# Kernel optimization log

Measured on AMD Instinct MI355X. Metric: run time of the kernel, lower is better.

Reference implementation:

```python
import jax, jax.numpy as jnp
import numpy as np

B, T, I, H = 256, 2048, 128, 128

def setup_inputs() -> dict:
    key = jax.random.key(0)
    k = jax.random.split(key, 5)
    bound = 1.0 / np.sqrt(H)  # torch RNNCell init: U(-1/sqrt(H), 1/sqrt(H))
    return {
        "x": jax.random.normal(k[0], (B, T, I), dtype=jnp.float32),
        "weight_ih": jax.random.uniform(k[1], (H, I), jnp.float32, -bound, bound),
        "weight_hh": jax.random.uniform(k[2], (H, H), jnp.float32, -bound, bound),
        "bias_ih": jax.random.uniform(k[3], (H,), jnp.float32, -bound, bound),
        "bias_hh": jax.random.uniform(k[4], (H,), jnp.float32, -bound, bound),
    }

def reference(x, weight_ih, weight_hh, bias_ih, bias_hh):
    # Tanh RNN: h_t = tanh(x_t @ W_ih^T + b_ih + h_{t-1} @ W_hh^T + b_hh)
    # Precompute the input projection for all timesteps (one big GEMM),
    # then scan the recurrent part (sequential dependency on h).
    b = x.shape[0]
    h0 = jnp.zeros((b, weight_hh.shape[0]), dtype=x.dtype)
    # [B, T, H]
    x_proj = jnp.einsum('bti,hi->bth', x, weight_ih) + bias_ih + bias_hh

    def step(h, xt):  # xt: [B, H]
        h_new = jnp.tanh(xt + h @ weight_hh.T)
        return h_new, h_new

    _, out = jax.lax.scan(step, h0, jnp.swapaxes(x_proj, 0, 1))  # out: [T, B, H]
    return jnp.swapaxes(out, 0, 1)  # [B, T, H]
```

## Files before the change

### kernel.cpp

```cpp
#include <hip/hip_runtime.h>

#define BB 256
#define TT 2048
#define II 128
#define HH 128
#define GS 16
#define NG (TT / GS)

typedef __attribute__((ext_vector_type(8))) short short8;
typedef __attribute__((ext_vector_type(4))) float f32x4;

__device__ __forceinline__ void step_barrier() {
    asm volatile("s_waitcnt lgkmcnt(0)\n\ts_barrier" ::: "memory");
}

__device__ __forceinline__ float tanh_fast(float s) {
#if __has_builtin(__builtin_amdgcn_exp2f)
    const float e = __builtin_amdgcn_exp2f(s * 2.8853900817779268f);
#else
    const float e = exp2f(s * 2.8853900817779268f);
#endif
    return 1.0f - 2.0f * __builtin_amdgcn_rcpf(e + 1.0f);
}

__device__ __forceinline__ unsigned int f2bf(float f) {
    unsigned int u = __float_as_uint(f);
    u += 0x7FFF + ((u >> 16) & 1);
    return u >> 16;
}
__device__ __forceinline__ unsigned int cvtpk(float a, float b) {
    unsigned int r;
    asm("v_cvt_pk_bf16_f32 %0, %1, %2" : "=v"(r) : "v"(a), "v"(b));
    return r;
}

__launch_bounds__(512, 1)
__global__ void rnn_pipe(const float* __restrict__ x,
                         const float* __restrict__ w_ih,
                         const float* __restrict__ w_hh,
                         const float* __restrict__ b_ih,
                         const float* __restrict__ b_hh,
                         float* __restrict__ out) {
    const int b    = blockIdx.x;
    const int tid  = threadIdx.x;
    const int wave = tid >> 6;
    const int lane = tid & 63;
    const bool hw  = (wave < 4);

    __shared__ __align__(16) unsigned short hA[2][HH];
    __shared__ __align__(16) float axbuf[3][GS][HH];
    __shared__ __align__(16) unsigned short xstage[2][4][64][8];

    const float* xb = x + (size_t)b * (TT * II);
    const f32x4 z4 = {0.f, 0.f, 0.f, 0.f};

    const int jb_h = (wave & 3) * 32;
    short8 WH[2][4];
    if (hw) {
#pragma unroll
        for (int nt = 0; nt < 2; ++nt) {
            const int jj = jb_h + nt * 16 + (lane & 15);
#pragma unroll
            for (int kf = 0; kf < 4; ++kf) {
                short8 s;
#pragma unroll
                for (int e = 0; e < 8; ++e) {
                    const int kp = kf * 32 + (lane >> 4) * 8 + e;
                    const int mm = kp & 31;
                    const int ko = (kp & ~31) + (mm >> 1) + ((mm & 1) << 4);
                    s[e] = (short)f2bf(w_hh[(size_t)jj * HH + ko]);
                }
                WH[nt][kf] = s;
            }
        }
    }

    const int xwq = wave - 4;
    const int jb  = xwq * 32;
    short8 WF[2][4];
    float biasv[2];
    f32x4 bs0 = z4, bs1 = z4;
    const int q   = tid - 256;
    const int t_s = q >> 4;
    const int m   = q & 15;
    const int i0  = m * 8;
    const int kfs = m >> 2;
    const int lps = (m & 3) * 16 + t_s;
    const int c16 = lane & 15;
    if (!hw) {
#pragma unroll
        for (int nt = 0; nt < 2; ++nt) {
            const int jj = jb + nt * 16 + (lane & 15);
            biasv[nt] = b_ih[jj] + b_hh[jj];
#pragma unroll
            for (int kf = 0; kf < 4; ++kf) {
                const float* wp = w_ih + (size_t)jj * II + kf * 32 + (lane >> 4) * 8;
                short8 s;
#pragma unroll
                for (int e = 0; e < 8; ++e) s[e] = (short)f2bf(wp[e]);
                WF[nt][kf] = s;
            }
        }
#pragma unroll
        for (int r = 0; r < 4; ++r) { bs0[r] = biasv[0]; bs1[r] = biasv[1]; }
    }

#define STAGE_X(BUF, R0, R1) do { \
        uint4 P_; \
        P_.x = cvtpk((R0).x, (R0).y); P_.y = cvtpk((R0).z, (R0).w); \
        P_.z = cvtpk((R1).x, (R1).y); P_.w = cvtpk((R1).z, (R1).w); \
        *reinterpret_cast<uint4*>(&xstage[BUF][kfs][lps][0]) = P_; } while (0)

#define XPROJ(SB, AB) do { \
        const short8 PA0 = *reinterpret_cast<const short8*>(&xstage[SB][0][lane][0]); \
        const short8 PA1 = *reinterpret_cast<const short8*>(&xstage[SB][1][lane][0]); \
        const short8 PA2 = *reinterpret_cast<const short8*>(&xstage[SB][2][lane][0]); \
        const short8 PA3 = *reinterpret_cast<const short8*>(&xstage[SB][3][lane][0]); \
        f32x4 ac0 = z4, ac1 = z4; \
        ac0 = __builtin_amdgcn_mfma_f32_16x16x32_bf16(PA0, WF[0][0], ac0, 0, 0, 0); \
        ac0 = __builtin_amdgcn_mfma_f32_16x16x32_bf16(PA1, WF[0][1], ac0, 0, 0, 0); \
        ac0 = __builtin_amdgcn_mfma_f32_16x16x32_bf16(PA2, WF[0][2], ac0, 0, 0, 0); \
        ac0 = __builtin_amdgcn_mfma_f32_16x16x32_bf16(PA3, WF[0][3], ac0, 0, 0, 0); \
        ac1 = __builtin_amdgcn_mfma_f32_16x16x32_bf16(PA0, WF[1][0], ac1, 0, 0, 0); \
        ac1 = __builtin_amdgcn_mfma_f32_16x16x32_bf16(PA1, WF[1][1], ac1, 0, 0, 0); \
        ac1 = __builtin_amdgcn_mfma_f32_16x16x32_bf16(PA2, WF[1][2], ac1, 0, 0, 0); \
        ac1 = __builtin_amdgcn_mfma_f32_16x16x32_bf16(PA3, WF[1][3], ac1, 0, 0, 0); \
        const int c_ = lane & 15, rb_ = (lane >> 4) * 4; \
        _Pragma("unroll") \
        for (int r = 0; r < 4; ++r) { \
            axbuf[AB][rb_ + r][jb + c_]      = ac0[r] + biasv[0]; \
            axbuf[AB][rb_ + r][jb + 16 + c_] = ac1[r] + biasv[1]; \
        } } while (0)

    float4 nr0, nr1;
    if (!hw) {
        float4 p0 = *reinterpret_cast<const float4*>(&xb[t_s * II + i0]);
        float4 p1 = *reinterpret_cast<const float4*>(&xb[t_s * II + i0 + 4]);
        STAGE_X(0, p0, p1);
    }
    if (tid < HH) hA[0][tid] = 0;
    __syncthreads();
    if (!hw) XPROJ(0, 0);
    __syncthreads();
    if (!hw) {
        float4 p0 = *reinterpret_cast<const float4*>(&xb[(GS + t_s) * II + i0]);
        float4 p1 = *reinterpret_cast<const float4*>(&xb[(GS + t_s) * II + i0 + 4]);
        STAGE_X(0, p0, p1);
    }
    __syncthreads();
    if (!hw) XPROJ(0, 1);
    __syncthreads();
    if (!hw) {
        float4 p0 = *reinterpret_cast<const float4*>(&xb[(2 * GS + t_s) * II + i0]);
        float4 p1 = *reinterpret_cast<const float4*>(&xb[(2 * GS + t_s) * II + i0 + 4]);
        STAGE_X(0, p0, p1);
        nr0 = *reinterpret_cast<const float4*>(&xb[(size_t)(3 * GS + t_s) * II + i0]);
        nr1 = *reinterpret_cast<const float4*>(&xb[(size_t)(3 * GS + t_s) * II + i0 + 4]);
    }
    __syncthreads();

    float axn0 = 0.f, axn1 = 0.f;
    f32x4 d00 = z4, d10 = z4;
    if (hw) {
        axn0 = axbuf[0][0][jb_h + c16];
        axn1 = axbuf[0][0][jb_h + 16 + c16];
        __builtin_amdgcn_s_setprio(1);
    }

    float* xout = nullptr;
    if (!hw && lane < 32) {
        xout = out + (size_t)b * (TT * HH) + jb + c16 + ((lane & 16) ? 16 : 0);
    }

    for (int g = 0; g < NG; ++g) {
        const int g3  = g % 3;
        const int g3n = (g + 1) % 3;
        const int g3x = (g + 2) % 3;
#pragma unroll
        for (int w = 0; w < GS; ++w) {
            if (hw) {
                const int p  = w & 1;
                const int ko = (lane >> 4) * 8;
                const short8 A0 = *reinterpret_cast<const short8*>(&hA[p][ 0 + ko]);
                const short8 A1 = *reinterpret_cast<const short8*>(&hA[p][32 + ko]);
                const short8 A2 = *reinterpret_cast<const short8*>(&hA[p][64 + ko]);
                const short8 A3 = *reinterpret_cast<const short8*>(&hA[p][96 + ko]);
                d00[0] = axn0;
                d10[0] = axn1;
                f32x4 e01, e02, e03, e11, e12, e13;
                d00 = __builtin_amdgcn_mfma_f32_16x16x32_bf16(A0, WH[0][0], d00, 0, 0, 0);
                e01 = __builtin_amdgcn_mfma_f32_16x16x32_bf16(A1, WH[0][1], z4,  0, 0, 0);
                e02 = __builtin_amdgcn_mfma_f32_16x16x32_bf16(A2, WH[0][2], z4,  0, 0, 0);
                e03 = __builtin_amdgcn_mfma_f32_16x16x32_bf16(A3, WH[0][3], z4,  0, 0, 0);
                d10 = __builtin_amdgcn_mfma_f32_16x16x32_bf16(A0, WH[1][0], d10, 0, 0, 0);
                e11 = __builtin_amdgcn_mfma_f32_16x16x32_bf16(A1, WH[1][1], z4,  0, 0, 0);
                e12 = __builtin_amdgcn_mfma_f32_16x16x32_bf16(A2, WH[1][2], z4,  0, 0, 0);
                e13 = __builtin_amdgcn_mfma_f32_16x16x32_bf16(A3, WH[1][3], z4,  0, 0, 0);
                {
                    const int wn  = (w + 1) & (GS - 1);
                    const int gnb = (w == GS - 1) ? g3n : g3;
                    axn0 = axbuf[gnb][wn][jb_h + c16];
                    axn1 = axbuf[gnb][wn][jb_h + 16 + c16];
                }
                const float s0 = (d00[0] + e01[0]) + (e02[0] + e03[0]);
                const float s1 = (d10[0] + e11[0]) + (e12[0] + e13[0]);
                const float hn0 = tanh_fast(s0);
                const float hn1 = tanh_fast(s1);
                const unsigned int hpk = cvtpk(hn0, hn1);
                if (lane < 16) {
                    *reinterpret_cast<unsigned int*>(&hA[p ^ 1][jb_h + 2 * lane]) = hpk;
                }
            } else {
                const int T = (g << 4) + w;
                if (T != 0 && lane < 32) {
                    const unsigned int rd = *reinterpret_cast<const unsigned int*>(
                        &hA[w & 1][jb + 2 * c16]);
                    const unsigned int v = (lane & 16) ? (rd & 0xffff0000u) : (rd << 16);
                    xout[(size_t)(T - 1) * HH] = __uint_as_float(v);
                }
                if (w == 14) {
                    if (g + 2 < NG) {
                        const short8 XA0 = *reinterpret_cast<const short8*>(&xstage[g & 1][0][lane][0]);
                        const short8 XA1 = *reinterpret_cast<const short8*>(&xstage[g & 1][1][lane][0]);
                        const short8 XA2 = *reinterpret_cast<const short8*>(&xstage[g & 1][2][lane][0]);
                        const short8 XA3 = *reinterpret_cast<const short8*>(&xstage[g & 1][3][lane][0]);
                        f32x4 xp0, xp1, xp2, xp3, yp0, yp1, yp2, yp3;
                        xp0 = __builtin_amdgcn_mfma_f32_16x16x32_bf16(XA0, WF[0][0], bs0, 0, 0, 0);
                        yp0 = __builtin_amdgcn_mfma_f32_16x16x32_bf16(XA0, WF[1][0], bs1, 0, 0, 0);
                        xp1 = __builtin_amdgcn_mfma_f32_16x16x32_bf16(XA1, WF[0][1], z4, 0, 0, 0);
                        yp1 = __builtin_amdgcn_mfma_f32_16x16x32_bf16(XA1, WF[1][1], z4, 0, 0, 0);
                        xp2 = __builtin_amdgcn_mfma_f32_16x16x32_bf16(XA2, WF[0][2], z4, 0, 0, 0);
                        yp2 = __builtin_amdgcn_mfma_f32_16x16x32_bf16(XA2, WF[1][2], z4, 0, 0, 0);
                        xp3 = __builtin_amdgcn_mfma_f32_16x16x32_bf16(XA3, WF[0][3], z4, 0, 0, 0);
                        yp3 = __builtin_amdgcn_mfma_f32_16x16x32_bf16(XA3, WF[1][3], z4, 0, 0, 0);
                        const f32x4 t0 = (xp0 + xp1) + (xp2 + xp3);
                        const f32x4 t1 = (yp0 + yp1) + (yp2 + yp3);
                        const int c_ = lane & 15, rb_ = (lane >> 4) * 4;
#pragma unroll
                        for (int r = 0; r < 4; ++r) {
                            axbuf[g3x][rb_ + r][jb + c_]      = t0[r];
                            axbuf[g3x][rb_ + r][jb + 16 + c_] = t1[r];
                        }
                    }
                    if (g + 3 < NG) {
                        STAGE_X((g + 1) & 1, nr0, nr1);
                    }
                    if (g + 4 < NG) {
                        const int tb = (g + 4) * GS;
                        nr0 = *reinterpret_cast<const float4*>(&xb[(size_t)(tb + t_s) * II + i0]);
                        nr1 = *reinterpret_cast<const float4*>(&xb[(size_t)(tb + t_s) * II + i0 + 4]);
                    }
                }
            }
            step_barrier();
        }
    }

    if (!hw && lane < 32) {
        const unsigned int rd = *reinterpret_cast<const unsigned int*>(
            &hA[0][jb + 2 * c16]);
        const unsigned int v = (lane & 16) ? (rd & 0xffff0000u) : (rd << 16);
        xout[(size_t)(TT - 1) * HH] = __uint_as_float(v);
    }
#undef XPROJ
#undef STAGE_X
}

extern "C" void kernel_launch(void* const* d_in, const int* in_sizes, int n_in,
                              void* d_out, int out_size, void* d_ws, size_t ws_size,
                              hipStream_t stream) {
    const float* x    = (const float*)d_in[0];
    const float* w_ih = (const float*)d_in[1];
    const float* w_hh = (const float*)d_in[2];
    const float* b_ih = (const float*)d_in[3];
    const float* b_hh = (const float*)d_in[4];
    float* out = (float*)d_out;

    rnn_pipe<<<BB, 512, 0, stream>>>(x, w_ih, w_hh, b_ih, b_hh, out);
}
```

Before: 464.7 us.

## Replicate hidden-state LDS buffer per row group and shrink projection pipeline depth

The hidden-state buffer is replicated four times, once per 16-lane row group, with padding. All lanes now write their packed bf16 h values into their own replica, and each row group reads only its own copy. The aim is to reduce LDS bank conflicts and broadcast contention on the serial recurrence's critical path. The x-projection ring buffer also shrinks from three to two stages, with the prologue and prefetch distances adjusted to match; this saves LDS but leaves less slack between the projection producer and the recurrent consumer.

```diff
diff --git a/kernel.cpp b/kernel.cpp
--- a/kernel.cpp
+++ b/kernel.cpp
@@ -6,6 +6,7 @@
 #define HH 128
 #define GS 16
 #define NG (TT / GS)
+#define HREP (HH + 8)
 
 typedef __attribute__((ext_vector_type(8))) short short8;
 typedef __attribute__((ext_vector_type(4))) float f32x4;
@@ -47,8 +48,8 @@
     const int lane = tid & 63;
     const bool hw  = (wave < 4);
 
-    __shared__ __align__(16) unsigned short hA[2][HH];
-    __shared__ __align__(16) float axbuf[3][GS][HH];
+    __shared__ __align__(16) unsigned short hAr[4][2][HREP];
+    __shared__ __align__(16) float axbuf[2][GS][HH];
     __shared__ __align__(16) unsigned short xstage[2][4][64][8];
 
     const float* xb = x + (size_t)b * (TT * II);
@@ -87,6 +88,7 @@
     const int kfs = m >> 2;
     const int lps = (m & 3) * 16 + t_s;
     const int c16 = lane & 15;
+    const int rg  = lane >> 4;
     if (!hw) {
 #pragma unroll
         for (int nt = 0; nt < 2; ++nt) {
@@ -136,26 +138,18 @@
     if (!hw) {
         float4 p0 = *reinterpret_cast<const float4*>(&xb[t_s * II + i0]);
         float4 p1 = *reinterpret_cast<const float4*>(&xb[t_s * II + i0 + 4]);
-        STAGE_X(0, p0, p1);
-    }
-    if (tid < HH) hA[0][tid] = 0;
-    __syncthreads();
-    if (!hw) XPROJ(0, 0);
+        STAGE_X(1, p0, p1);
+    }
+    for (int i = tid; i < 4 * 2 * HREP; i += 512)
+        ((unsigned short*)hAr)[i] = 0;
     __syncthreads();
     if (!hw) {
+        XPROJ(1, 0);
         float4 p0 = *reinterpret_cast<const float4*>(&xb[(GS + t_s) * II + i0]);
         float4 p1 = *reinterpret_cast<const float4*>(&xb[(GS + t_s) * II + i0 + 4]);
         STAGE_X(0, p0, p1);
-    }
-    __syncthreads();
-    if (!hw) XPROJ(0, 1);
-    __syncthreads();
-    if (!hw) {
-        float4 p0 = *reinterpret_cast<const float4*>(&xb[(2 * GS + t_s) * II + i0]);
-        float4 p1 = *reinterpret_cast<const float4*>(&xb[(2 * GS + t_s) * II + i0 + 4]);
-        STAGE_X(0, p0, p1);
-        nr0 = *reinterpret_cast<const float4*>(&xb[(size_t)(3 * GS + t_s) * II + i0]);
-        nr1 = *reinterpret_cast<const float4*>(&xb[(size_t)(3 * GS + t_s) * II + i0 + 4]);
+        nr0 = *reinterpret_cast<const float4*>(&xb[(size_t)(2 * GS + t_s) * II + i0]);
+        nr1 = *reinterpret_cast<const float4*>(&xb[(size_t)(2 * GS + t_s) * II + i0 + 4]);
     }
     __syncthreads();
 
@@ -173,18 +167,15 @@
     }
 
     for (int g = 0; g < NG; ++g) {
-        const int g3  = g % 3;
-        const int g3n = (g + 1) % 3;
-        const int g3x = (g + 2) % 3;
 #pragma unroll
         for (int w = 0; w < GS; ++w) {
             if (hw) {
                 const int p  = w & 1;
-                const int ko = (lane >> 4) * 8;
-                const short8 A0 = *reinterpret_cast<const short8*>(&hA[p][ 0 + ko]);
-                const short8 A1 = *reinterpret_cast<const short8*>(&hA[p][32 + ko]);
-                const short8 A2 = *reinterpret_cast<const short8*>(&hA[p][64 + ko]);
-                const short8 A3 = *reinterpret_cast<const short8*>(&hA[p][96 + ko]);
+                const int ko = rg * 8;
+                const short8 A0 = *reinterpret_cast<const short8*>(&hAr[rg][p][ 0 + ko]);
+                const short8 A1 = *reinterpret_cast<const short8*>(&hAr[rg][p][32 + ko]);
+                const short8 A2 = *reinterpret_cast<const short8*>(&hAr[rg][p][64 + ko]);
+                const short8 A3 = *reinterpret_cast<const short8*>(&hAr[rg][p][96 + ko]);
                 d00[0] = axn0;
                 d10[0] = axn1;
                 f32x4 e01, e02, e03, e11, e12, e13;
@@ -198,7 +189,7 @@
                 e13 = __builtin_amdgcn_mfma_f32_16x16x32_bf16(A3, WH[1][3], z4,  0, 0, 0);
                 {
                     const int wn  = (w + 1) & (GS - 1);
-                    const int gnb = (w == GS - 1) ? g3n : g3;
+                    const int gnb = (w == GS - 1) ? ((g + 1) & 1) : (g & 1);
                     axn0 = axbuf[gnb][wn][jb_h + c16];
                     axn1 = axbuf[gnb][wn][jb_h + 16 + c16];
                 }
@@ -207,19 +198,17 @@
                 const float hn0 = tanh_fast(s0);
                 const float hn1 = tanh_fast(s1);
                 const unsigned int hpk = cvtpk(hn0, hn1);
-                if (lane < 16) {
-                    *reinterpret_cast<unsigned int*>(&hA[p ^ 1][jb_h + 2 * lane]) = hpk;
-                }
+                *reinterpret_cast<unsigned int*>(&hAr[rg][p ^ 1][jb_h + 2 * c16]) = hpk;
             } else {
                 const int T = (g << 4) + w;
                 if (T != 0 && lane < 32) {
                     const unsigned int rd = *reinterpret_cast<const unsigned int*>(
-                        &hA[w & 1][jb + 2 * c16]);
+                        &hAr[0][w & 1][jb + 2 * c16]);
                     const unsigned int v = (lane & 16) ? (rd & 0xffff0000u) : (rd << 16);
                     xout[(size_t)(T - 1) * HH] = __uint_as_float(v);
                 }
                 if (w == 14) {
-                    if (g + 2 < NG) {
+                    if (g + 1 < NG) {
                         const short8 XA0 = *reinterpret_cast<const short8*>(&xstage[g & 1][0][lane][0]);
                         const short8 XA1 = *reinterpret_cast<const short8*>(&xstage[g & 1][1][lane][0]);
                         const short8 XA2 = *reinterpret_cast<const short8*>(&xstage[g & 1][2][lane][0]);
@@ -238,15 +227,15 @@
                         const int c_ = lane & 15, rb_ = (lane >> 4) * 4;
 #pragma unroll
                         for (int r = 0; r < 4; ++r) {
-                            axbuf[g3x][rb_ + r][jb + c_]      = t0[r];
-                            axbuf[g3x][rb_ + r][jb + 16 + c_] = t1[r];
+                            axbuf[(g + 1) & 1][rb_ + r][jb + c_]      = t0[r];
+                            axbuf[(g + 1) & 1][rb_ + r][jb + 16 + c_] = t1[r];
                         }
                     }
-                    if (g + 3 < NG) {
+                    if (g + 2 < NG) {
                         STAGE_X((g + 1) & 1, nr0, nr1);
                     }
-                    if (g + 4 < NG) {
-                        const int tb = (g + 4) * GS;
+                    if (g + 3 < NG) {
+                        const int tb = (g + 3) * GS;
                         nr0 = *reinterpret_cast<const float4*>(&xb[(size_t)(tb + t_s) * II + i0]);
                         nr1 = *reinterpret_cast<const float4*>(&xb[(size_t)(tb + t_s) * II + i0 + 4]);
                     }
@@ -258,7 +247,7 @@
 
     if (!hw && lane < 32) {
         const unsigned int rd = *reinterpret_cast<const unsigned int*>(
-            &hA[0][jb + 2 * c16]);
+            &hAr[0][0][jb + 2 * c16]);
         const unsigned int v = (lane & 16) ? (rd & 0xffff0000u) : (rd << 16);
         xout[(size_t)(TT - 1) * HH] = __uint_as_float(v);
     }
```

After: 532.0 us. 1.14x slower.
